# Kernel tuning notes

Measured on AMD Instinct MI355X. Metric: run time of the kernel, lower is better.

## Reference

```python
import jax, jax.numpy as jnp
import numpy as np

# Model dims (match init_kwargs)
D_MODEL = 2048
H = 16        # query heads
HKV = 4       # kv heads (GQA)
DS = 32       # semantic head dim (compressed)
DG = 32       # geometric head dim (compressed, RoPE'd)
DV = 64       # value head dim
B, T = 2, 4096
MB = 64       # mem_block
LW = 1024     # local_window
ROPE_BASE = 10000.0
NEG_INF = -1e9


def _rope(x, pos, base):
    # x: [B, h, T, d] with d even; standard rotate-half RoPE
    d = x.shape[-1]
    inv_freq = 1.0 / (base ** (jnp.arange(0, d, 2, dtype=jnp.float32) / d))
    ang = pos.astype(jnp.float32)[:, None] * inv_freq          # [T, d/2]
    cos, sin = jnp.cos(ang), jnp.sin(ang)                      # [T, d/2]
    x1, x2 = jnp.split(x, 2, axis=-1)
    return jnp.concatenate([x1 * cos - x2 * sin,
                            x2 * cos + x1 * sin], axis=-1)


def setup_inputs() -> dict:
    key = jax.random.key(0)
    ks = jax.random.split(key, 8)
    w = lambda k, sh: jax.random.normal(k, sh, jnp.float32) * 0.02
    return {
        "x": jax.random.normal(ks[0], (B, T, D_MODEL), jnp.float32),
        "Wq_sem": w(ks[1], (D_MODEL, H * DS)),
        "Wk_sem": w(ks[2], (D_MODEL, HKV * DS)),
        "Wq_geo": w(ks[3], (D_MODEL, H * DG)),
        "Wk_geo": w(ks[4], (D_MODEL, HKV * DG)),
        "Wv": w(ks[5], (D_MODEL, HKV * DV)),
        "Wo": w(ks[6], (H * DV, D_MODEL)),
        "logit_scale": jnp.zeros((H,), jnp.float32),
    }


def reference(x, Wq_sem, Wk_sem, Wq_geo, Wk_geo, Wv, Wo, logit_scale):
    Bq, Tq = x.shape[0], x.shape[1]
    split = lambda y, h, d: y.reshape(Bq, Tq, h, d).transpose(0, 2, 1, 3)
    # Decoupled projections
    q_sem = split(x @ Wq_sem, H, DS)      # [B,H,T,DS]
    k_sem = split(x @ Wk_sem, HKV, DS)    # [B,HKV,T,DS]
    q_geo = split(x @ Wq_geo, H, DG)
    k_geo = split(x @ Wk_geo, HKV, DG)
    v = split(x @ Wv, HKV, DV)            # [B,HKV,T,DV]
    pos = jnp.arange(Tq)
    # RoPE only on the geometric path
    q_geo = _rope(q_geo, pos, ROPE_BASE)
    k_geo = _rope(k_geo, pos, ROPE_BASE)
    # Memory-block summarization: mean-pool remote KV into one token per block
    remote = Tq - LW
    nblk = remote // MB
    pool = lambda a: jnp.concatenate(
        [a[:, :, :remote].reshape(Bq, HKV, nblk, MB, a.shape[-1]).mean(axis=3),
         a[:, :, remote:]], axis=2)
    k_sem2, k_geo2, v2 = pool(k_sem), pool(k_geo), pool(v)  # [B,HKV,K,*], K=nblk+LW
    k_pos = jnp.concatenate([jnp.arange(nblk) * MB + (MB - 1),
                             jnp.arange(remote, Tq)])        # [K]
    # GQA head-group broadcast
    rep = lambda a: jnp.repeat(a, H // HKV, axis=1)
    k_sem2, k_geo2, v2 = rep(k_sem2), rep(k_geo2), rep(v2)   # [B,H,K,*]
    # Decoupled scores: semantic + geometric, each with its own scale
    scores = (jnp.einsum('bhqd,bhkd->bhqk', q_sem, k_sem2) * (1.0 / jnp.sqrt(float(DS)))
              + jnp.einsum('bhqd,bhkd->bhqk', q_geo, k_geo2) * (1.0 / jnp.sqrt(float(DG))))
    # Learned per-head temperature
    scores = scores * jnp.exp(logit_scale)[None, :, None, None]
    # Causal mask over summarized key positions
    mask = k_pos[None, :] <= pos[:, None]                    # [T,K]
    scores = jnp.where(mask[None, None], scores, NEG_INF)
    probs = jax.nn.softmax(scores, axis=-1)
    out = jnp.einsum('bhqk,bhkd->bhqd', probs, v2)           # [B,H,T,DV]
    out = out.transpose(0, 2, 1, 3).reshape(Bq, Tq, H * DV)
    return out @ Wo                                          # [B,T,D_MODEL]
```

## Files before the change

### kernel.cpp

```cpp
#include <hip/hip_runtime.h>
#include <math.h>

#define B_  2
#define T_  4096
#define DM  2048
#define H_  16
#define HKV 4
#define DV_ 64
#define MB_ 64
#define LW_ 1024
#define REMOTE 3072
#define NBLK 48
#define KTOT 1072
#define NTILES 17

typedef __bf16 bf16x8 __attribute__((ext_vector_type(8)));
typedef float  f32x4  __attribute__((ext_vector_type(4)));

__device__ __forceinline__ float bf2f(unsigned short u) {
    unsigned int x = ((unsigned int)u) << 16;
    return __builtin_bit_cast(float, x);
}
__device__ __forceinline__ unsigned short f2bf(float f) {
    unsigned int x = __builtin_bit_cast(unsigned int, f);
    x = x + 0x7fffu + ((x >> 16) & 1u);
    return (unsigned short)(x >> 16);
}

__device__ __forceinline__ void gload16(const unsigned short* gsrc,
                                        unsigned short* ldst) {
    __builtin_amdgcn_global_load_lds(
        (const __attribute__((address_space(1))) void*)gsrc,
        (__attribute__((address_space(3))) void*)ldst,
        16, 0, 0);
}

__global__ void cvt_f32_to_bf16(const float* __restrict__ src,
                                unsigned short* __restrict__ dst, int n4) {
    int stride = gridDim.x * blockDim.x;
    for (int i = blockIdx.x * blockDim.x + threadIdx.x; i < n4; i += stride) {
        float4 v = ((const float4*)src)[i];
        ushort4 o = make_ushort4(f2bf(v.x), f2bf(v.y), f2bf(v.z), f2bf(v.w));
        ((ushort4*)dst)[i] = o;
    }
}

__global__ void transpose_all(const float* __restrict__ Wq_sem,
                              const float* __restrict__ Wq_geo,
                              const float* __restrict__ Wk_sem,
                              const float* __restrict__ Wk_geo,
                              const float* __restrict__ Wv,
                              const float* __restrict__ Wo,
                              unsigned short* __restrict__ WcatT,
                              unsigned short* __restrict__ WoT) {
    __shared__ float tile[32][33];
    const int bid = blockIdx.x;
    const float* src; unsigned short* dst; int R, C, tiles_x, lt;
    if (bid < 1024)      { src = Wq_sem; dst = WcatT;                       R = 2048; C = 512;  tiles_x = 16; lt = bid; }
    else if (bid < 2048) { src = Wq_geo; dst = WcatT + (size_t)512  * 2048; R = 2048; C = 512;  tiles_x = 16; lt = bid - 1024; }
    else if (bid < 2304) { src = Wk_sem; dst = WcatT + (size_t)1024 * 2048; R = 2048; C = 128;  tiles_x = 4;  lt = bid - 2048; }
    else if (bid < 2560) { src = Wk_geo; dst = WcatT + (size_t)1152 * 2048; R = 2048; C = 128;  tiles_x = 4;  lt = bid - 2304; }
    else if (bid < 3072) { src = Wv;     dst = WcatT + (size_t)1280 * 2048; R = 2048; C = 256;  tiles_x = 8;  lt = bid - 2560; }
    else                 { src = Wo;     dst = WoT;                         R = 1024; C = 2048; tiles_x = 64; lt = bid - 3072; }
    const int ct = lt % tiles_x, rt = lt / tiles_x;
    const int tx = threadIdx.x, ty = threadIdx.y;
    #pragma unroll
    for (int i = ty; i < 32; i += 8)
        tile[i][tx] = src[(size_t)(rt * 32 + i) * C + ct * 32 + tx];
    __syncthreads();
    #pragma unroll
    for (int i = ty; i < 32; i += 8)
        dst[(size_t)(ct * 32 + i) * R + rt * 32 + tx] = f2bf(tile[tx][i]);
}

template<int MODE>
__global__ __launch_bounds__(256, MODE == 1 ? 4 : 3) void gemmP(
    const unsigned short* __restrict__ A,
    const unsigned short* __restrict__ BT,
    float* __restrict__ outF,
    unsigned short* __restrict__ qcat,
    unsigned short* __restrict__ kp,
    unsigned short* __restrict__ vt,
    int M, int N, int K, int nbx)
{
    constexpr int RING = (MODE == 1) ? 2 : 3;
    extern __shared__ __align__(16) unsigned short lds[];

    const int tid = threadIdx.x;
    const int lane = tid & 63, w = tid >> 6;
    const int wr = w >> 1, wc = w & 1;
    const int l15 = lane & 15, lg = lane >> 4;

    const int cpx = gridDim.x >> 3;
    const int swz = (blockIdx.x & 7) * cpx + (blockIdx.x >> 3);
    const int bx = swz % nbx, by = swz / nbx;
    const int row0 = by * 128, col0 = bx * 128;

    const int scol = ((lane & 3) ^ ((lane >> 3) & 3)) * 8;
    const int srA = w * 16 + (lane >> 2);
    const unsigned short* Ag = A  + (size_t)row0 * K;
    const unsigned short* Bg = BT + (size_t)col0 * K;

    const int rdsw = (lg ^ ((l15 >> 1) & 3)) * 8;
    const int aoff = (wr * 64 + l15) * 32 + rdsw;
    const int boff = (wc * 64 + l15) * 32 + rdsw;

    const int NT = K >> 5;
    f32x4 acc[4][4] = {};

    auto stage = [&](int s, int kk) {
        unsigned short* sa = lds + s * 8192;
        unsigned short* sb = sa + 4096;
        #pragma unroll
        for (int j = 0; j < 2; j++) {
            gload16(Ag + (size_t)(srA + j * 64) * K + kk + scol,
                    sa + (j * 256 + w * 64) * 8);
            gload16(Bg + (size_t)(srA + j * 64) * K + kk + scol,
                    sb + (j * 256 + w * 64) * 8);
        }
    };

    if (RING == 3) {
        stage(0, 0);
        stage(1, 32);
        asm volatile("s_waitcnt vmcnt(4)" ::: "memory");
    } else {
        stage(0, 0);
        asm volatile("s_waitcnt vmcnt(0)" ::: "memory");
    }

    int rs = 0;
    for (int t = 0; t < NT; ++t) {
        __builtin_amdgcn_s_barrier();
        if (RING == 3) {
            if (t + 2 < NT) stage(rs == 0 ? 2 : rs - 1, (t + 2) << 5);
        } else {
            if (t + 1 < NT) stage(rs ^ 1, (t + 1) << 5);
        }

        const unsigned short* As_ = lds + rs * 8192;
        const unsigned short* Bs_ = As_ + 4096;
        bf16x8 af[4], bfr[4];
        #pragma unroll
        for (int mf = 0; mf < 4; mf++)
            af[mf] = __builtin_bit_cast(bf16x8, *(const uint4*)&As_[aoff + mf * 512]);
        #pragma unroll
        for (int nf = 0; nf < 4; nf++)
            bfr[nf] = __builtin_bit_cast(bf16x8, *(const uint4*)&Bs_[boff + nf * 512]);

        __builtin_amdgcn_s_setprio(1);
        #pragma unroll
        for (int mf = 0; mf < 4; mf++)
            #pragma unroll
            for (int nf = 0; nf < 4; nf++)
                acc[mf][nf] = __builtin_amdgcn_mfma_f32_16x16x32_bf16(
                                  af[mf], bfr[nf], acc[mf][nf], 0, 0, 0);
        __builtin_amdgcn_s_setprio(0);

        if (RING == 3) {
            if (t + 2 < NT) asm volatile("s_waitcnt vmcnt(4)" ::: "memory");
            else            asm volatile("s_waitcnt vmcnt(0)" ::: "memory");
            rs = (rs == 2) ? 0 : rs + 1;
        } else {
            if (t + 1 < NT) asm volatile("s_waitcnt vmcnt(0)" ::: "memory");
            rs ^= 1;
        }
    }

    if (MODE == 1) {
        #pragma unroll
        for (int mf = 0; mf < 4; mf++)
            #pragma unroll
            for (int nf = 0; nf < 4; nf++)
                #pragma unroll
                for (int r = 0; r < 4; r++) {
                    int row = row0 + wr * 64 + mf * 16 + lg * 4 + r;
                    int col = col0 + wc * 64 + nf * 16 + l15;
                    outF[(size_t)row * N + col] = acc[mf][nf][r];
                }
    } else {
        const int cspan = col0 + wc * 64;
        const int tbase = row0 & 4095;
        const int bq = row0 >> 12;

        if ((cspan >= 512 && cspan < 1024) || (cspan >= 1152 && cspan < 1280)) {
            const float invf = exp2f(-(float)l15 * 0.8304820237218406f);
            #pragma unroll
            for (int mf = 0; mf < 4; mf++) {
                #pragma unroll
                for (int r = 0; r < 4; r++) {
                    float s, c;
                    sincosf((float)(tbase + wr*64 + mf*16 + lg*4 + r) * invf, &s, &c);
                    float a0 = acc[mf][0][r], a1 = acc[mf][1][r];
                    acc[mf][0][r] = a0 * c - a1 * s;
                    acc[mf][1][r] = a1 * c + a0 * s;
                    float a2 = acc[mf][2][r], a3 = acc[mf][3][r];
                    acc[mf][2][r] = a2 * c - a3 * s;
                    acc[mf][3][r] = a3 * c + a2 * s;
                }
            }
        }

        if (cspan < 1024) {
            #pragma unroll
            for (int nf = 0; nf < 4; nf++) {
                int col = cspan + nf * 16 + l15;
                int h = (col < 512) ? (col >> 5) : ((col - 512) >> 5);
                int d = (col < 512) ? (col & 31) : (32 + (col & 31));
                unsigned short* qb =
                    qcat + (((size_t)(bq * 16 + h)) * 4096 + tbase) * 64 + d;
                #pragma unroll
                for (int mf = 0; mf < 4; mf++)
                    #pragma unroll
                    for (int r = 0; r < 4; r++)
                        qb[(size_t)(wr*64 + mf*16 + lg*4 + r) * 64] =
                            f2bf(acc[mf][nf][r]);
            }
        } else if (tbase >= REMOTE) {
            #pragma unroll
            for (int nf = 0; nf < 4; nf++) {
                int col = cspan + nf * 16 + l15;
                #pragma unroll
                for (int mf = 0; mf < 4; mf++)
                    #pragma unroll
                    for (int r = 0; r < 4; r++) {
                        int key = tbase + wr*64 + mf*16 + lg*4 + r - 3024;
                        unsigned short hv = f2bf(acc[mf][nf][r]);
                        if (col < 1280) {
                            int g, dk;
                            if (col < 1152) { g = (col - 1024) >> 5; dk = col & 31; }
                            else            { g = (col - 1152) >> 5; dk = 32 + (col & 31); }
                            kp[(((size_t)(bq*4 + g)) * KTOT + key) * 64 + dk] = hv;
                        } else {
                            int g = (col - 1280) >> 6, dv = col & 63;
                            vt[(((size_t)(bq*4 + g)) * 64 + dv) * KTOT + key] = hv;
                        }
                    }
            }
        } else {
            #pragma unroll
            for (int nf = 0; nf < 4; nf++) {
                float ps = 0.f;
                #pragma unroll
                for (int mf = 0; mf < 4; mf++)
                    #pragma unroll
                    for (int r = 0; r < 4; r++) ps += acc[mf][nf][r];
                ps += __shfl_xor(ps, 16);
                ps += __shfl_xor(ps, 32);
                if (lane < 16) {
                    int col = cspan + nf * 16 + l15;
                    int key = (tbase >> 6) + wr;
                    unsigned short hv = f2bf(ps * (1.f / 64.f));
                    if (col < 1280) {
                        int g, dk;
                        if (col < 1152) { g = (col - 1024) >> 5; dk = col & 31; }
                        else            { g = (col - 1152) >> 5; dk = 32 + (col & 31); }
                        kp[(((size_t)(bq*4 + g)) * KTOT + key) * 64 + dk] = hv;
                    } else {
                        int g = (col - 1280) >> 6, dv = col & 63;
                        vt[(((size_t)(bq*4 + g)) * 64 + dv) * KTOT + key] = hv;
                    }
                }
            }
        }
    }
}

__global__ __launch_bounds__(256) void attn_fwd(
    const unsigned short* __restrict__ qcat,
    const unsigned short* __restrict__ kp,
    const unsigned short* __restrict__ vt,
    const float* __restrict__ ls,
    unsigned short* __restrict__ attn_out)
{
    __shared__ unsigned short Pl[4][32][72];

    const int tid = threadIdx.x;
    const int lane = tid & 63, w = tid >> 6;
    const int l15 = lane & 15, lg = lane >> 4;

    const int wid = blockIdx.x * 4 + w;
    const int hb = wid & 31;
    const int iu = wid >> 5;
    int i;
    if (iu < 32)       i = 127 - iu;
    else if (iu == 32) i = 0;
    else if (iu == 33) i = 1;
    else               i = iu - 32;
    const int h = hb & 15, b = hb >> 4, g = h >> 2;
    const int q0 = i * 32;

    int ktmax;
    if (q0 < 64) ktmax = NTILES;
    else {
        int lastkey = q0 + 31 - 3024;
        ktmax = (lastkey < NBLK) ? 1 : (lastkey / 64 + 1);
    }

    const float sc = __expf(ls[h]) * 0.17677669529663687f;

    bf16x8 aq[2][2];
    const unsigned short* qbase = qcat + (((size_t)(b * 16 + h)) * T_ + q0) * 64;
    #pragma unroll
    for (int rf = 0; rf < 2; rf++)
        #pragma unroll
        for (int kh = 0; kh < 2; kh++)
            aq[rf][kh] = __builtin_bit_cast(bf16x8,
                *(const uint4*)(qbase + (size_t)(rf*16 + l15)*64 + kh*32 + lg*8));

    float m[2][4], lrun[2][4];
    #pragma unroll
    for (int rf = 0; rf < 2; rf++)
        #pragma unroll
        for (int r = 0; r < 4; r++) { m[rf][r] = -1e9f; lrun[rf][r] = 0.f; }
    f32x4 oacc[2][4] = {};

    const unsigned short* kbase = kp + ((size_t)(b * 4 + g)) * KTOT * 64;
    const unsigned short* vbase = vt + ((size_t)(b * 4 + g)) * 64 * KTOT;

    for (int kt = 0; kt < ktmax; kt++) {
        const int kb = kt * 64;

        bf16x8 bk[4][2];
        #pragma unroll
        for (int nf = 0; nf < 4; nf++) {
            int krow = kb + nf*16 + l15;
            int krc = krow < KTOT ? krow : KTOT - 1;
            #pragma unroll
            for (int kh = 0; kh < 2; kh++)
                bk[nf][kh] = __builtin_bit_cast(bf16x8,
                    *(const uint4*)(kbase + (size_t)krc * 64 + kh*32 + lg*8));
        }

        f32x4 s[2][4] = {};
        #pragma unroll
        for (int rf = 0; rf < 2; rf++)
            #pragma unroll
            for (int nf = 0; nf < 4; nf++)
                #pragma unroll
                for (int kh = 0; kh < 2; kh++)
                    s[rf][nf] = __builtin_amdgcn_mfma_f32_16x16x32_bf16(
                                    aq[rf][kh], bk[nf][kh], s[rf][nf], 0, 0, 0);

        bf16x8 bv[4][2];
        #pragma unroll
        for (int nfv = 0; nfv < 4; nfv++)
            #pragma unroll
            for (int kh = 0; kh < 2; kh++) {
                int kc = kb + kh*32 + lg*8;
                int kcc = (kc + 8 <= KTOT) ? kc : KTOT - 8;
                bv[nfv][kh] = __builtin_bit_cast(bf16x8,
                    *(const uint4*)(vbase + (size_t)(nfv*16 + l15) * KTOT + kcc));
            }

        #pragma unroll
        for (int rf = 0; rf < 2; rf++) {
            #pragma unroll
            for (int r = 0; r < 4; r++) {
                const int qpos = q0 + rf*16 + lg*4 + r;
                float vals[4];
                float tmax = -INFINITY;
                #pragma unroll
                for (int nf = 0; nf < 4; nf++) {
                    int key = kb + nf*16 + l15;
                    float v = s[rf][nf][r] * sc;
                    int kpos = (key < NBLK) ? key * 64 + 63 : 3024 + key;
                    v = (key < KTOT) ? ((kpos <= qpos) ? v : -1e9f) : -INFINITY;
                    vals[nf] = v;
                    tmax = fmaxf(tmax, v);
                }
                #pragma unroll
                for (int d = 1; d < 16; d <<= 1)
                    tmax = fmaxf(tmax, __shfl_xor(tmax, d));
                float mn = fmaxf(m[rf][r], tmax);
                float scl = __expf(m[rf][r] - mn);
                m[rf][r] = mn;
                float rs = 0.f;
                #pragma unroll
                for (int nf = 0; nf < 4; nf++) {
                    unsigned short pb = f2bf(__expf(vals[nf] - mn));
                    rs += bf2f(pb);
                    Pl[w][rf*16 + lg*4 + r][nf*16 + l15] = pb;
                }
                #pragma unroll
                for (int d = 1; d < 16; d <<= 1)
                    rs += __shfl_xor(rs, d);
                lrun[rf][r] = lrun[rf][r] * scl + rs;
                #pragma unroll
                for (int nfv = 0; nfv < 4; nfv++)
                    oacc[rf][nfv][r] *= scl;
            }
        }

        #pragma unroll
        for (int rf = 0; rf < 2; rf++) {
            bf16x8 pa[2];
            #pragma unroll
            for (int kh = 0; kh < 2; kh++)
                pa[kh] = __builtin_bit_cast(bf16x8,
                    *(const uint4*)&Pl[w][rf*16 + l15][kh*32 + lg*8]);
            #pragma unroll
            for (int nfv = 0; nfv < 4; nfv++)
                #pragma unroll
                for (int kh = 0; kh < 2; kh++)
                    oacc[rf][nfv] = __builtin_amdgcn_mfma_f32_16x16x32_bf16(
                                        pa[kh], bv[nfv][kh], oacc[rf][nfv], 0, 0, 0);
        }
    }

    #pragma unroll
    for (int rf = 0; rf < 2; rf++) {
        #pragma unroll
        for (int r = 0; r < 4; r++) {
            float inv = 1.f / lrun[rf][r];
            int q = q0 + rf*16 + lg*4 + r;
            size_t obase = ((size_t)(b * T_ + q)) * 1024 + h * 64;
            #pragma unroll
            for (int nfv = 0; nfv < 4; nfv++)
                attn_out[obase + nfv*16 + l15] = f2bf(oacc[rf][nfv][r] * inv);
        }
    }
}

extern "C" void kernel_launch(void* const* d_in, const int* in_sizes, int n_in,
                              void* d_out, int out_size, void* d_ws, size_t ws_size,
                              hipStream_t stream) {
    const float* x      = (const float*)d_in[0];
    const float* Wq_sem = (const float*)d_in[1];
    const float* Wk_sem = (const float*)d_in[2];
    const float* Wq_geo = (const float*)d_in[3];
    const float* Wk_geo = (const float*)d_in[4];
    const float* Wv     = (const float*)d_in[5];
    const float* Wo     = (const float*)d_in[6];
    const float* ls     = (const float*)d_in[7];

    char* w = (char*)d_ws;
    auto alloc = [&](size_t bytes) {
        char* p = w;
        w += (bytes + 255) & ~(size_t)255;
        return p;
    };
    unsigned short* xb    = (unsigned short*)alloc((size_t)8192 * 2048 * 2);
    unsigned short* WcatT = (unsigned short*)alloc((size_t)1536 * 2048 * 2);
    unsigned short* WoT   = (unsigned short*)alloc((size_t)2048 * 1024 * 2);
    unsigned short* qcat  = (unsigned short*)alloc((size_t)2 * 16 * 4096 * 64 * 2);
    unsigned short* kp    = (unsigned short*)alloc((size_t)2 * 4 * 1072 * 64 * 2);
    unsigned short* vt    = (unsigned short*)alloc((size_t)2 * 4 * 1072 * 64 * 2);
    unsigned short* aout  = (unsigned short*)alloc((size_t)8192 * 1024 * 2);

    hipFuncSetAttribute(reinterpret_cast<const void*>(&gemmP<0>),
                        hipFuncAttributeMaxDynamicSharedMemorySize, 49152);
    hipFuncSetAttribute(reinterpret_cast<const void*>(&gemmP<1>),
                        hipFuncAttributeMaxDynamicSharedMemorySize, 32768);

    cvt_f32_to_bf16<<<2048, 256, 0, stream>>>(x, xb, 8192 * 2048 / 4);

    transpose_all<<<5120, dim3(32, 8), 0, stream>>>(
        Wq_sem, Wq_geo, Wk_sem, Wk_geo, Wv, Wo, WcatT, WoT);

    gemmP<0><<<768, 256, 49152, stream>>>(
        xb, WcatT, nullptr, qcat, kp, vt, 8192, 1536, 2048, 12);

    attn_fwd<<<dim3(1024), 256, 0, stream>>>(qcat, kp, vt, ls, aout);

    gemmP<1><<<1024, 256, 32768, stream>>>(
        aout, WoT, (float*)d_out, nullptr, nullptr, nullptr, 8192, 2048, 1024, 16);
}
```

Baseline: 193.5 us.

## Fuse fp32-to-bf16 conversion of x into projection GEMM A-tile loads

```diff
diff --git a/kernel.cpp b/kernel.cpp
--- a/kernel.cpp
+++ b/kernel.cpp
@@ -27,22 +27,11 @@
     return (unsigned short)(x >> 16);
 }
 
-__device__ __forceinline__ void gload16(const unsigned short* gsrc,
-                                        unsigned short* ldst) {
+__device__ __forceinline__ void gload16(const void* gsrc, unsigned short* ldst) {
     __builtin_amdgcn_global_load_lds(
         (const __attribute__((address_space(1))) void*)gsrc,
         (__attribute__((address_space(3))) void*)ldst,
         16, 0, 0);
-}
-
-__global__ void cvt_f32_to_bf16(const float* __restrict__ src,
-                                unsigned short* __restrict__ dst, int n4) {
-    int stride = gridDim.x * blockDim.x;
-    for (int i = blockIdx.x * blockDim.x + threadIdx.x; i < n4; i += stride) {
-        float4 v = ((const float4*)src)[i];
-        ushort4 o = make_ushort4(f2bf(v.x), f2bf(v.y), f2bf(v.z), f2bf(v.w));
-        ((ushort4*)dst)[i] = o;
-    }
 }
 
 __global__ void transpose_all(const float* __restrict__ Wq_sem,
@@ -74,8 +63,8 @@
 }
 
 template<int MODE>
-__global__ __launch_bounds__(256, MODE == 1 ? 4 : 3) void gemmP(
-    const unsigned short* __restrict__ A,
+__global__ __launch_bounds__(256, 3) void gemmP(
+    const void* __restrict__ Ap,
     const unsigned short* __restrict__ BT,
     float* __restrict__ outF,
     unsigned short* __restrict__ qcat,
@@ -83,7 +72,8 @@
     unsigned short* __restrict__ vt,
     int M, int N, int K, int nbx)
 {
-    constexpr int RING = (MODE == 1) ? 2 : 3;
+    constexpr int RING = (MODE == 0) ? 2 : 3;
+    constexpr int SLOT = (MODE == 0) ? 12288 : 8192;
     extern __shared__ __align__(16) unsigned short lds[];
 
     const int tid = threadIdx.x;
@@ -98,25 +88,44 @@
 
     const int scol = ((lane & 3) ^ ((lane >> 3) & 3)) * 8;
     const int srA = w * 16 + (lane >> 2);
-    const unsigned short* Ag = A  + (size_t)row0 * K;
     const unsigned short* Bg = BT + (size_t)col0 * K;
 
+    const float* Agf = (const float*)Ap + (size_t)row0 * K;
+    const int arow0 = tid >> 3;
+    const int alc4  = ((tid & 7) ^ (arow0 & 7)) * 4;
+    const unsigned short* Agh = (const unsigned short*)Ap + (size_t)row0 * K;
+
     const int rdsw = (lg ^ ((l15 >> 1) & 3)) * 8;
-    const int aoff = (wr * 64 + l15) * 32 + rdsw;
     const int boff = (wc * 64 + l15) * 32 + rdsw;
+    const int aoff_h = (wr * 64 + l15) * 32 + rdsw;
+    const int aoff_f = (wr * 64 + l15) * 32;
+    const int c0f = ((lg * 2)     ^ (l15 & 7)) * 4;
+    const int c1f = ((lg * 2 + 1) ^ (l15 & 7)) * 4;
 
     const int NT = K >> 5;
     f32x4 acc[4][4] = {};
 
     auto stage = [&](int s, int kk) {
-        unsigned short* sa = lds + s * 8192;
-        unsigned short* sb = sa + 4096;
-        #pragma unroll
-        for (int j = 0; j < 2; j++) {
-            gload16(Ag + (size_t)(srA + j * 64) * K + kk + scol,
-                    sa + (j * 256 + w * 64) * 8);
-            gload16(Bg + (size_t)(srA + j * 64) * K + kk + scol,
-                    sb + (j * 256 + w * 64) * 8);
+        unsigned short* sa = lds + s * SLOT;
+        if (MODE == 0) {
+            unsigned short* sb = sa + 8192;
+            #pragma unroll
+            for (int s4 = 0; s4 < 4; s4++)
+                gload16(Agf + (size_t)(arow0 + s4 * 32) * K + kk + alc4,
+                        sa + (s4 * 256 + w * 64) * 8);
+            #pragma unroll
+            for (int j = 0; j < 2; j++)
+                gload16(Bg + (size_t)(srA + j * 64) * K + kk + scol,
+                        sb + (j * 256 + w * 64) * 8);
+        } else {
+            unsigned short* sb = sa + 4096;
+            #pragma unroll
+            for (int j = 0; j < 2; j++) {
+                gload16(Agh + (size_t)(srA + j * 64) * K + kk + scol,
+                        sa + (j * 256 + w * 64) * 8);
+                gload16(Bg + (size_t)(srA + j * 64) * K + kk + scol,
+                        sb + (j * 256 + w * 64) * 8);
+            }
         }
     };
 
@@ -138,15 +147,34 @@
             if (t + 1 < NT) stage(rs ^ 1, (t + 1) << 5);
         }
 
-        const unsigned short* As_ = lds + rs * 8192;
-        const unsigned short* Bs_ = As_ + 4096;
         bf16x8 af[4], bfr[4];
-        #pragma unroll
-        for (int mf = 0; mf < 4; mf++)
-            af[mf] = __builtin_bit_cast(bf16x8, *(const uint4*)&As_[aoff + mf * 512]);
-        #pragma unroll
-        for (int nf = 0; nf < 4; nf++)
-            bfr[nf] = __builtin_bit_cast(bf16x8, *(const uint4*)&Bs_[boff + nf * 512]);
+        if (MODE == 0) {
+            const float* Asf = (const float*)(lds + rs * SLOT);
+            const unsigned short* Bs_ = lds + rs * SLOT + 8192;
+            #pragma unroll
+            for (int mf = 0; mf < 4; mf++) {
+                float4 f0 = *(const float4*)&Asf[aoff_f + mf * 512 + c0f];
+                float4 f1 = *(const float4*)&Asf[aoff_f + mf * 512 + c1f];
+                bf16x8 a;
+                a[0] = (__bf16)f0.x; a[1] = (__bf16)f0.y;
+                a[2] = (__bf16)f0.z; a[3] = (__bf16)f0.w;
+                a[4] = (__bf16)f1.x; a[5] = (__bf16)f1.y;
+                a[6] = (__bf16)f1.z; a[7] = (__bf16)f1.w;
+                af[mf] = a;
+            }
+            #pragma unroll
+            for (int nf = 0; nf < 4; nf++)
+                bfr[nf] = __builtin_bit_cast(bf16x8, *(const uint4*)&Bs_[boff + nf * 512]);
+        } else {
+            const unsigned short* As_ = lds + rs * SLOT;
+            const unsigned short* Bs_ = As_ + 4096;
+            #pragma unroll
+            for (int mf = 0; mf < 4; mf++)
+                af[mf] = __builtin_bit_cast(bf16x8, *(const uint4*)&As_[aoff_h + mf * 512]);
+            #pragma unroll
+            for (int nf = 0; nf < 4; nf++)
+                bfr[nf] = __builtin_bit_cast(bf16x8, *(const uint4*)&Bs_[boff + nf * 512]);
+        }
 
         __builtin_amdgcn_s_setprio(1);
         #pragma unroll
@@ -440,7 +468,6 @@
         w += (bytes + 255) & ~(size_t)255;
         return p;
     };
-    unsigned short* xb    = (unsigned short*)alloc((size_t)8192 * 2048 * 2);
     unsigned short* WcatT = (unsigned short*)alloc((size_t)1536 * 2048 * 2);
     unsigned short* WoT   = (unsigned short*)alloc((size_t)2048 * 1024 * 2);
     unsigned short* qcat  = (unsigned short*)alloc((size_t)2 * 16 * 4096 * 64 * 2);
@@ -451,18 +478,16 @@
     hipFuncSetAttribute(reinterpret_cast<const void*>(&gemmP<0>),
                         hipFuncAttributeMaxDynamicSharedMemorySize, 49152);
     hipFuncSetAttribute(reinterpret_cast<const void*>(&gemmP<1>),
-                        hipFuncAttributeMaxDynamicSharedMemorySize, 32768);
-
-    cvt_f32_to_bf16<<<2048, 256, 0, stream>>>(x, xb, 8192 * 2048 / 4);
+                        hipFuncAttributeMaxDynamicSharedMemorySize, 49152);
 
     transpose_all<<<5120, dim3(32, 8), 0, stream>>>(
         Wq_sem, Wq_geo, Wk_sem, Wk_geo, Wv, Wo, WcatT, WoT);
 
     gemmP<0><<<768, 256, 49152, stream>>>(
-        xb, WcatT, nullptr, qcat, kp, vt, 8192, 1536, 2048, 12);
+        x, WcatT, nullptr, qcat, kp, vt, 8192, 1536, 2048, 12);
 
     attn_fwd<<<dim3(1024), 256, 0, stream>>>(qcat, kp, vt, ls, aout);
 
-    gemmP<1><<<1024, 256, 32768, stream>>>(
+    gemmP<1><<<1024, 256, 49152, stream>>>(
         aout, WoT, (float*)d_out, nullptr, nullptr, nullptr, 8192, 2048, 1024, 16);
 }
```

Measured after the change: 186.6 us. 1.04x faster.

## Fuse fp32-to-bf16 conversion of x into QKV projection GEMM A-tile loading

Applied to the files above, without the earlier changes.

```diff
diff --git a/kernel.cpp b/kernel.cpp
--- a/kernel.cpp
+++ b/kernel.cpp
@@ -27,22 +27,11 @@
     return (unsigned short)(x >> 16);
 }
 
-__device__ __forceinline__ void gload16(const unsigned short* gsrc,
-                                        unsigned short* ldst) {
+__device__ __forceinline__ void gload16(const void* gsrc, unsigned short* ldst) {
     __builtin_amdgcn_global_load_lds(
         (const __attribute__((address_space(1))) void*)gsrc,
         (__attribute__((address_space(3))) void*)ldst,
         16, 0, 0);
-}
-
-__global__ void cvt_f32_to_bf16(const float* __restrict__ src,
-                                unsigned short* __restrict__ dst, int n4) {
-    int stride = gridDim.x * blockDim.x;
-    for (int i = blockIdx.x * blockDim.x + threadIdx.x; i < n4; i += stride) {
-        float4 v = ((const float4*)src)[i];
-        ushort4 o = make_ushort4(f2bf(v.x), f2bf(v.y), f2bf(v.z), f2bf(v.w));
-        ((ushort4*)dst)[i] = o;
-    }
 }
 
 __global__ void transpose_all(const float* __restrict__ Wq_sem,
@@ -74,8 +63,8 @@
 }
 
 template<int MODE>
-__global__ __launch_bounds__(256, MODE == 1 ? 4 : 3) void gemmP(
-    const unsigned short* __restrict__ A,
+__global__ __launch_bounds__(256, 3) void gemmP(
+    const void* __restrict__ Ap,
     const unsigned short* __restrict__ BT,
     float* __restrict__ outF,
     unsigned short* __restrict__ qcat,
@@ -83,7 +72,6 @@
     unsigned short* __restrict__ vt,
     int M, int N, int K, int nbx)
 {
-    constexpr int RING = (MODE == 1) ? 2 : 3;
     extern __shared__ __align__(16) unsigned short lds[];
 
     const int tid = threadIdx.x;
@@ -98,8 +86,13 @@
 
     const int scol = ((lane & 3) ^ ((lane >> 3) & 3)) * 8;
     const int srA = w * 16 + (lane >> 2);
-    const unsigned short* Ag = A  + (size_t)row0 * K;
     const unsigned short* Bg = BT + (size_t)col0 * K;
+    const unsigned short* Agh = (const unsigned short*)Ap + (size_t)row0 * K;
+
+    const int ar0 = tid >> 2, ar1 = ar0 + 64, ac = tid & 3;
+    const int agc0 = (ac ^ ((ar0 >> 1) & 3)) * 8;
+    const int agc1 = (ac ^ ((ar1 >> 1) & 3)) * 8;
+    const float* Axf = (const float*)Ap + (size_t)row0 * K;
 
     const int rdsw = (lg ^ ((l15 >> 1) & 3)) * 8;
     const int aoff = (wr * 64 + l15) * 32 + rdsw;
@@ -108,64 +101,125 @@
     const int NT = K >> 5;
     f32x4 acc[4][4] = {};
 
-    auto stage = [&](int s, int kk) {
+    auto stageB = [&](int s, int kk) {
+        unsigned short* sb = lds + s * 8192 + 4096;
+        #pragma unroll
+        for (int j = 0; j < 2; j++)
+            gload16(Bg + (size_t)(srA + j * 64) * K + kk + scol,
+                    sb + (j * 256 + w * 64) * 8);
+    };
+    auto stageAB = [&](int s, int kk) {
         unsigned short* sa = lds + s * 8192;
         unsigned short* sb = sa + 4096;
         #pragma unroll
         for (int j = 0; j < 2; j++) {
-            gload16(Ag + (size_t)(srA + j * 64) * K + kk + scol,
+            gload16(Agh + (size_t)(srA + j * 64) * K + kk + scol,
                     sa + (j * 256 + w * 64) * 8);
             gload16(Bg + (size_t)(srA + j * 64) * K + kk + scol,
                     sb + (j * 256 + w * 64) * 8);
         }
     };
-
-    if (RING == 3) {
-        stage(0, 0);
-        stage(1, 32);
+    auto issueA = [&](float4* ra, int kk) {
+        ra[0] = *(const float4*)&Axf[(size_t)ar0 * K + kk + agc0];
+        ra[1] = *(const float4*)&Axf[(size_t)ar0 * K + kk + agc0 + 4];
+        ra[2] = *(const float4*)&Axf[(size_t)ar1 * K + kk + agc1];
+        ra[3] = *(const float4*)&Axf[(size_t)ar1 * K + kk + agc1 + 4];
+    };
+    auto writeA = [&](int s, const float4* ra) {
+        unsigned short* sa = lds + s * 8192;
+        bf16x8 v0, v1;
+        v0[0] = (__bf16)ra[0].x; v0[1] = (__bf16)ra[0].y;
+        v0[2] = (__bf16)ra[0].z; v0[3] = (__bf16)ra[0].w;
+        v0[4] = (__bf16)ra[1].x; v0[5] = (__bf16)ra[1].y;
+        v0[6] = (__bf16)ra[1].z; v0[7] = (__bf16)ra[1].w;
+        v1[0] = (__bf16)ra[2].x; v1[1] = (__bf16)ra[2].y;
+        v1[2] = (__bf16)ra[2].z; v1[3] = (__bf16)ra[2].w;
+        v1[4] = (__bf16)ra[3].x; v1[5] = (__bf16)ra[3].y;
+        v1[6] = (__bf16)ra[3].z; v1[7] = (__bf16)ra[3].w;
+        *(uint4*)&sa[ar0 * 32 + ac * 8] = __builtin_bit_cast(uint4, v0);
+        *(uint4*)&sa[ar1 * 32 + ac * 8] = __builtin_bit_cast(uint4, v1);
+    };
+
+    #define FRAGS_MFMA(rs_)                                                     \
+        {                                                                       \
+            const unsigned short* As_ = lds + (rs_) * 8192;                     \
+            const unsigned short* Bs_ = As_ + 4096;                             \
+            bf16x8 af[4], bfr[4];                                               \
+            _Pragma("unroll")                                                   \
+            for (int mf = 0; mf < 4; mf++)                                      \
+                af[mf] = __builtin_bit_cast(bf16x8,                             \
+                    *(const uint4*)&As_[aoff + mf * 512]);                      \
+            _Pragma("unroll")                                                   \
+            for (int nf = 0; nf < 4; nf++)                                      \
+                bfr[nf] = __builtin_bit_cast(bf16x8,                            \
+                    *(const uint4*)&Bs_[boff + nf * 512]);                      \
+            __builtin_amdgcn_s_setprio(1);                                      \
+            _Pragma("unroll")                                                   \
+            for (int mf = 0; mf < 4; mf++)                                      \
+                _Pragma("unroll")                                               \
+                for (int nf = 0; nf < 4; nf++)                                  \
+                    acc[mf][nf] = __builtin_amdgcn_mfma_f32_16x16x32_bf16(      \
+                        af[mf], bfr[nf], acc[mf][nf], 0, 0, 0);                 \
+            __builtin_amdgcn_s_setprio(0);                                      \
+        }
+
+    if (MODE == 0) {
+        stageB(0, 0);
+        stageB(1, 32);
+        __builtin_amdgcn_sched_barrier(0);
+        float4 rA[4], rB[4];
+        issueA(rA, 0);
+        issueA(rB, 32);
+        writeA(0, rA);
+        asm volatile("s_waitcnt lgkmcnt(0)" ::: "memory");
+        __builtin_amdgcn_s_barrier();
+
+        int rs = 0;
+        for (int t = 0; t < NT; t += 2) {
+            {
+                if (t + 2 < NT) {
+                    stageB(rs == 0 ? 2 : rs - 1, (t + 2) << 5);
+                    __builtin_amdgcn_sched_barrier(0);
+                    issueA(rA, (t + 2) << 5);
+                }
+                FRAGS_MFMA(rs);
+                int s1 = (rs == 2) ? 0 : rs + 1;
+                writeA(s1, rB);
+                asm volatile("s_waitcnt vmcnt(6)" ::: "memory");
+                asm volatile("s_waitcnt lgkmcnt(0)" ::: "memory");
+                __builtin_amdgcn_s_barrier();
+                rs = s1;
+            }
+            {
+                if (t + 3 < NT) {
+                    stageB(rs == 0 ? 2 : rs - 1, (t + 3) << 5);
+                    __builtin_amdgcn_sched_barrier(0);
+                    issueA(rB, (t + 3) << 5);
+                }
+                FRAGS_MFMA(rs);
+                int s1 = (rs == 2) ? 0 : rs + 1;
+                if (t + 2 < NT) writeA(s1, rA);
+                asm volatile("s_waitcnt vmcnt(6)" ::: "memory");
+                asm volatile("s_waitcnt lgkmcnt(0)" ::: "memory");
+                __builtin_amdgcn_s_barrier();
+                rs = s1;
+            }
+        }
+    } else {
+        stageAB(0, 0);
+        stageAB(1, 32);
         asm volatile("s_waitcnt vmcnt(4)" ::: "memory");
-    } else {
-        stage(0, 0);
-        asm volatile("s_waitcnt vmcnt(0)" ::: "memory");
-    }
-
-    int rs = 0;
-    for (int t = 0; t < NT; ++t) {
-        __builtin_amdgcn_s_barrier();
-        if (RING == 3) {
-            if (t + 2 < NT) stage(rs == 0 ? 2 : rs - 1, (t + 2) << 5);
-        } else {
-            if (t + 1 < NT) stage(rs ^ 1, (t + 1) << 5);
-        }
-
-        const unsigned short* As_ = lds + rs * 8192;
-        const unsigned short* Bs_ = As_ + 4096;
-        bf16x8 af[4], bfr[4];
-        #pragma unroll
-        for (int mf = 0; mf < 4; mf++)
-            af[mf] = __builtin_bit_cast(bf16x8, *(const uint4*)&As_[aoff + mf * 512]);
-        #pragma unroll
-        for (int nf = 0; nf < 4; nf++)
-            bfr[nf] = __builtin_bit_cast(bf16x8, *(const uint4*)&Bs_[boff + nf * 512]);
-
-        __builtin_amdgcn_s_setprio(1);
-        #pragma unroll
-        for (int mf = 0; mf < 4; mf++)
-            #pragma unroll
-            for (int nf = 0; nf < 4; nf++)
-                acc[mf][nf] = __builtin_amdgcn_mfma_f32_16x16x32_bf16(
-                                  af[mf], bfr[nf], acc[mf][nf], 0, 0, 0);
-        __builtin_amdgcn_s_setprio(0);
-
-        if (RING == 3) {
+        int rs = 0;
+        for (int t = 0; t < NT; ++t) {
+            __builtin_amdgcn_s_barrier();
+            if (t + 2 < NT) stageAB(rs == 0 ? 2 : rs - 1, (t + 2) << 5);
+            FRAGS_MFMA(rs);
             if (t + 2 < NT) asm volatile("s_waitcnt vmcnt(4)" ::: "memory");
             else            asm volatile("s_waitcnt vmcnt(0)" ::: "memory");
             rs = (rs == 2) ? 0 : rs + 1;
-        } else {
-            if (t + 1 < NT) asm volatile("s_waitcnt vmcnt(0)" ::: "memory");
-            rs ^= 1;
         }
     }
+    #undef FRAGS_MFMA
 
     if (MODE == 1) {
         #pragma unroll
@@ -440,7 +494,6 @@
         w += (bytes + 255) & ~(size_t)255;
         return p;
     };
-    unsigned short* xb    = (unsigned short*)alloc((size_t)8192 * 2048 * 2);
     unsigned short* WcatT = (unsigned short*)alloc((size_t)1536 * 2048 * 2);
     unsigned short* WoT   = (unsigned short*)alloc((size_t)2048 * 1024 * 2);
     unsigned short* qcat  = (unsigned short*)alloc((size_t)2 * 16 * 4096 * 64 * 2);
@@ -451,18 +504,16 @@
     hipFuncSetAttribute(reinterpret_cast<const void*>(&gemmP<0>),
                         hipFuncAttributeMaxDynamicSharedMemorySize, 49152);
     hipFuncSetAttribute(reinterpret_cast<const void*>(&gemmP<1>),
-                        hipFuncAttributeMaxDynamicSharedMemorySize, 32768);
-
-    cvt_f32_to_bf16<<<2048, 256, 0, stream>>>(x, xb, 8192 * 2048 / 4);
+                        hipFuncAttributeMaxDynamicSharedMemorySize, 49152);
 
     transpose_all<<<5120, dim3(32, 8), 0, stream>>>(
         Wq_sem, Wq_geo, Wk_sem, Wk_geo, Wv, Wo, WcatT, WoT);
 
     gemmP<0><<<768, 256, 49152, stream>>>(
-        xb, WcatT, nullptr, qcat, kp, vt, 8192, 1536, 2048, 12);
+        x, WcatT, nullptr, qcat, kp, vt, 8192, 1536, 2048, 12);
 
     attn_fwd<<<dim3(1024), 256, 0, stream>>>(qcat, kp, vt, ls, aout);
 
-    gemmP<1><<<1024, 256, 32768, stream>>>(
+    gemmP<1><<<1024, 256, 49152, stream>>>(
         aout, WoT, (float*)d_out, nullptr, nullptr, nullptr, 8192, 2048, 1024, 16);
 }
```

New measurement: 185.3 us. -4.2%, faster.
